# Performance work log

Measured on AMD Instinct MI355X. Metric: run time of the kernel, lower is better.

The kernel has to match this reference:

```python
import jax, jax.numpy as jnp
import numpy as np

N_NODES = 50000
N_EDGES = 800000
IN_FEATS = 32
OUT_FEATS = 32
NUM_HEADS = 4


def setup_inputs() -> dict:
    key = jax.random.key(0)
    ks = jax.random.split(key, 12)
    H, F, IN = NUM_HEADS, OUT_FEATS, IN_FEATS
    h = jax.random.normal(ks[0], (N_NODES, IN), dtype=jnp.float32)
    src = jax.random.randint(ks[1], (N_EDGES,), 0, N_NODES, dtype=jnp.int64)
    dst = jax.random.randint(ks[2], (N_EDGES,), 0, N_NODES, dtype=jnp.int64)
    s = 0.1
    W_gat = jax.random.normal(ks[3], (IN, H * F), dtype=jnp.float32) * s
    attn_l = jax.random.normal(ks[4], (H, F), dtype=jnp.float32) * s
    attn_r = jax.random.normal(ks[5], (H, F), dtype=jnp.float32) * s
    W_ih = jax.random.normal(ks[6], (3 * F, H * F), dtype=jnp.float32) * s
    W_hh = jax.random.normal(ks[7], (3 * F, F), dtype=jnp.float32) * s
    b_ih = jax.random.normal(ks[8], (3 * F,), dtype=jnp.float32) * s
    b_hh = jax.random.normal(ks[9], (3 * F,), dtype=jnp.float32) * s
    return {"h": h, "W_gat": W_gat, "attn_l": attn_l, "attn_r": attn_r,
            "W_ih": W_ih, "W_hh": W_hh, "b_ih": b_ih, "b_hh": b_hh,
            "src": src, "dst": dst}


def reference(h, W_gat, attn_l, attn_r, W_ih, W_hh, b_ih, b_hh, src, dst):
    N = h.shape[0]
    H, F = attn_l.shape
    # --- GATConv ---
    feat = (h @ W_gat).reshape(N, H, F)                      # (N,H,F)
    el = jnp.einsum('nhf,hf->nh', feat, attn_l)              # (N,H)
    er = jnp.einsum('nhf,hf->nh', feat, attn_r)              # (N,H)
    e = jax.nn.leaky_relu(el[src] + er[dst], 0.2)            # (E,H) edge logits
    emax = jax.ops.segment_max(e, dst, num_segments=N)       # per-dst max (stable)
    ee = jnp.exp(e - emax[dst])
    denom = jax.ops.segment_sum(ee, dst, num_segments=N)
    alpha = ee / denom[dst]                                  # segment softmax (E,H)
    msg = feat[src] * alpha[:, :, None]                      # (E,H,F)
    agg = jax.ops.segment_sum(msg, dst, num_segments=N)      # (N,H,F)
    x = agg.reshape(N, H * F)
    # --- GRUCell (torch semantics, gate order r,z,n) ---
    gi = x @ W_ih.T + b_ih                                   # (N,3F)
    gh = h @ W_hh.T + b_hh                                   # (N,3F)
    i_r, i_z, i_n = jnp.split(gi, 3, axis=1)
    h_r, h_z, h_n = jnp.split(gh, 3, axis=1)
    r = jax.nn.sigmoid(i_r + h_r)
    z = jax.nn.sigmoid(i_z + h_z)
    n = jnp.tanh(i_n + r * h_n)
    h_new = (1.0 - z) * n + z * h
    return jax.nn.elu(h_new)
```

## Files before the change

kernel.cpp:

```cpp
#include <hip/hip_runtime.h>
#include <hip/hip_bf16.h>
#include <cmath>

#define N_NODES 50000
#define N_EDGES 800000
#define CAP 64

#define NBINS 196
#define BIN_CAP 8192
#define CUR_PAD 32

#define WCB_ITEMS (144 * 32)
#define WCB_BLOCKS (WCB_ITEMS / 256)
#define WC_ITEMS (192 * 160)
#define WC_BLOCKS (WC_ITEMS / 256)

#define P1_EPT 8
#define P1_EPB (256 * P1_EPT)
#define P1_BLOCKS ((N_EDGES + P1_EPB - 1) / P1_EPB)
#define FEAT_BLOCKS ((N_NODES / 16 + 3) / 4)

typedef __attribute__((ext_vector_type(8))) short bf16x8;
typedef __attribute__((ext_vector_type(4))) float f32x4;

__device__ inline short bfbits(float x) {
    __hip_bfloat16 t = __float2bfloat16(x);
    return *reinterpret_cast<short*>(&t);
}

__device__ inline unsigned char f32_to_fp8(float x) {
    return (unsigned char)(__builtin_amdgcn_cvt_pk_fp8_f32(x, x, 0, false) & 0xff);
}

__global__ __launch_bounds__(256) void k_prep0(
        const float* __restrict__ Wg, const float* __restrict__ al,
        const float* __restrict__ ar, const float* __restrict__ Wih,
        const float* __restrict__ Whh, __hip_bfloat16* __restrict__ Wcomb,
        __hip_bfloat16* __restrict__ Wc, int* __restrict__ bin_cursor) {
    const int t = threadIdx.x;
    if (blockIdx.x < WCB_BLOCKS) {
        const int idx = blockIdx.x * 256 + t;
        const int row = idx >> 5, k = idx & 31;
        float v = 0.f;
        if (row < 128) {
            v = Wg[k * 128 + row];
        } else if (row < 136) {
            const int hd = (row - 128) & 3;
            const float* a = (row < 132) ? (al + hd * 32) : (ar + hd * 32);
            const float* w = Wg + k * 128 + hd * 32;
#pragma unroll
            for (int f = 0; f < 32; ++f) v = fmaf(w[f], a[f], v);
        }
        Wcomb[idx] = __float2bfloat16(v);
        return;
    }
    if (blockIdx.x < WCB_BLOCKS + WC_BLOCKS) {
        const int idx = (blockIdx.x - WCB_BLOCKS) * 256 + t;
        const int r = idx / 160, k = idx - r * 160;
        float v = 0.f;
        if (r < 96) { if (k < 128) v = Wih[r * 128 + k]; }
        else        { if (k >= 128) v = Whh[(r - 96) * 32 + (k - 128)]; }
        Wc[idx] = __float2bfloat16(v);
        return;
    }
    if (t < NBINS) bin_cursor[t * CUR_PAD] = 0;
}

__global__ __launch_bounds__(256) void k_part_feat(
        const float* __restrict__ h, const __hip_bfloat16* __restrict__ Wcomb,
        const int* __restrict__ src, const int* __restrict__ dst,
        int* __restrict__ bin_cursor, unsigned* __restrict__ bin_buf,
        unsigned char* __restrict__ feat, float* __restrict__ el,
        float* __restrict__ er) {
    const int t = threadIdx.x;
    if (blockIdx.x < P1_BLOCKS) {
        __shared__ int bcnt[256], bofs[256], cur[256], gbase[256];
        __shared__ int wt4[4];
        __shared__ unsigned stage[P1_EPB];
        bcnt[t] = 0;
        __syncthreads();
        int bn[P1_EPT];
        unsigned pk[P1_EPT];
        const int ebase = blockIdx.x * P1_EPB + t * P1_EPT;
        if (ebase < N_EDGES) {
            int dd[P1_EPT], ss[P1_EPT];
            *(int4*)(dd)     = *(const int4*)(dst + ebase);
            *(int4*)(dd + 4) = *(const int4*)(dst + ebase + 4);
            *(int4*)(ss)     = *(const int4*)(src + ebase);
            *(int4*)(ss + 4) = *(const int4*)(src + ebase + 4);
#pragma unroll
            for (int q = 0; q < P1_EPT; ++q) {
                bn[q] = dd[q] >> 8;
                pk[q] = (unsigned)ss[q] | ((unsigned)(dd[q] & 255) << 16);
                atomicAdd(&bcnt[bn[q]], 1);
            }
        } else {
#pragma unroll
            for (int q = 0; q < P1_EPT; ++q) bn[q] = -1;
        }
        __syncthreads();
        {
            const int wave = t >> 6, lane = t & 63;
            const int vv = bcnt[t];
            int x = vv;
#pragma unroll
            for (int m = 1; m < 64; m <<= 1) {
                const int y = __shfl_up(x, m, 64);
                if (lane >= m) x += y;
            }
            if (lane == 63) wt4[wave] = x;
            __syncthreads();
            int wb = 0;
#pragma unroll
            for (int i = 0; i < 4; ++i) if (i < wave) wb += wt4[i];
            const int off = wb + x - vv;
            bofs[t] = off;
            cur[t] = off;
            gbase[t] = (vv > 0) ? atomicAdd(&bin_cursor[t * CUR_PAD], vv) : 0;
        }
        __syncthreads();
#pragma unroll
        for (int q = 0; q < P1_EPT; ++q)
            if (bn[q] >= 0) stage[atomicAdd(&cur[bn[q]], 1)] = pk[q];
        __syncthreads();
        if (t < NBINS) {
            const int c = bcnt[t], o = bofs[t], g = gbase[t];
            unsigned* bb = bin_buf + (size_t)t * BIN_CAP;
            for (int j = 0; j < c; ++j) {
                const int gi = g + j;
                if (gi < BIN_CAP) bb[gi] = stage[o + j];
            }
        }
        return;
    }
    __shared__ unsigned char sbuf8[4][16][136];
    const int lane = t & 63, wave = t >> 6;
    const int li = lane & 15, quad = lane >> 4;
    const int mt = (blockIdx.x - P1_BLOCKS) * 4 + wave;
    if (mt >= N_NODES / 16) return;
    const int m_base = mt * 16;
    bf16x8 a;
    {
        const float4* hp = (const float4*)(h + (size_t)(m_base + li) * 32 + quad * 8);
        const float4 f0 = hp[0], f1 = hp[1];
        a[0] = bfbits(f0.x); a[1] = bfbits(f0.y); a[2] = bfbits(f0.z); a[3] = bfbits(f0.w);
        a[4] = bfbits(f1.x); a[5] = bfbits(f1.y); a[6] = bfbits(f1.z); a[7] = bfbits(f1.w);
    }
    f32x4 acc[9];
#pragma unroll
    for (int j = 0; j < 9; ++j) acc[j] = (f32x4){0.f, 0.f, 0.f, 0.f};
#pragma unroll
    for (int j = 0; j < 9; ++j) {
        const bf16x8 b = *(const bf16x8*)(Wcomb + (size_t)(j * 16 + li) * 32 + quad * 8);
        acc[j] = __builtin_amdgcn_mfma_f32_16x16x32_bf16(a, b, acc[j], 0, 0, 0);
    }
#pragma unroll
    for (int j = 0; j < 8; ++j)
#pragma unroll
        for (int i = 0; i < 4; ++i)
            sbuf8[wave][quad * 4 + i][j * 16 + li] = f32_to_fp8(acc[j][i]);
    __builtin_amdgcn_wave_barrier();
#pragma unroll
    for (int rep = 0; rep < 4; ++rep) {
        const int row = rep * 4 + quad;
        const unsigned long long v = *(const unsigned long long*)(&sbuf8[wave][row][li * 8]);
        *(unsigned long long*)(feat + (size_t)(m_base + row) * 128 + li * 8) = v;
    }
    if (li < 8) {
#pragma unroll
        for (int i = 0; i < 4; ++i) {
            const int m = m_base + quad * 4 + i;
            if (li < 4) el[m * 4 + li] = acc[8][i];
            else        er[m * 4 + (li - 4)] = acc[8][i];
        }
    }
}

__global__ __launch_bounds__(256) void k_scat2(
        const int* __restrict__ bin_cursor, const unsigned* __restrict__ bin_buf,
        int* __restrict__ srcs_p, int* __restrict__ counts) {
    __shared__ int lcnt[256];
    const int t = threadIdx.x;
    const int b = blockIdx.x;
    lcnt[t] = 0;
    __syncthreads();
    const int cb = min(bin_cursor[b * CUR_PAD], BIN_CAP);
    const uint4* bb4 = (const uint4*)(bin_buf + (size_t)b * BIN_CAP);
    for (int i = t * 4; i < cb; i += 1024) {
        const uint4 p4 = bb4[i >> 2];
#pragma unroll
        for (int k = 0; k < 4; ++k) {
            if (i + k < cb) {
                const unsigned p = (&p4.x)[k];
                const int dl = p >> 16;
                const int s = p & 0xffff;
                const int pos = atomicAdd(&lcnt[dl], 1);
                if (pos < CAP) srcs_p[(size_t)(b * 256 + dl) * CAP + pos] = s;
            }
        }
    }
    __syncthreads();
    const int node = b * 256 + t;
    if (node < N_NODES) counts[node] = lcnt[t];
}

__global__ __launch_bounds__(256) void k_aggr_gru(
        const int* __restrict__ counts, const int* __restrict__ srcs_p,
        const unsigned char* __restrict__ feat,
        const float* __restrict__ el, const float* __restrict__ er,
        const float* __restrict__ h, const __hip_bfloat16* __restrict__ Wc,
        const float* __restrict__ bih, const float* __restrict__ bhh,
        float* __restrict__ out) {
    __shared__ __hip_bfloat16 xh_tile[16][160];
    __shared__ int   sl_s[4][4][64];
    __shared__ float eel_s[4][256];
    __shared__ float ex[2][3][16][16];
    const int wave = threadIdx.x >> 6;
    const int lane = threadIdx.x & 63;
    float* eel = eel_s[wave];
    const int hs = lane & 3;
    const int eh = lane >> 5;
    const int fl = lane & 31;
    const int hq = fl >> 3;
    const int mbase = blockIdx.x * 16;

    int cnts[4];
#pragma unroll
    for (int u = 0; u < 4; ++u) {
        const int n = mbase + wave * 4 + u;
        cnts[u] = min(counts[n], CAP);
        if (lane < cnts[u]) sl_s[wave][u][lane] = srcs_p[(size_t)n * CAP + lane];
    }
    __builtin_amdgcn_wave_barrier();
    for (int u = 0; u < 4; ++u) {
        const int row = wave * 4 + u;
        const int n = mbase + row;
        const float ern = er[n * 4 + hs];
        const int cnt = cnts[u];
        const int* sl = sl_s[wave][u];
        float a0 = 0.f, a1 = 0.f, a2 = 0.f, a3 = 0.f, psum = 0.f;
#pragma unroll
        for (int p = 0; p < 4; ++p) {
            const int j = p * 64 + lane;
            if (j < cnt * 4) {
                const int s = sl[j >> 2];
                float v = el[s * 4 + hs] + ern;
                v = v > 0.f ? v : 0.2f * v;
                const float e = expf(v);
                eel[j] = e;
                psum += e;
            }
        }
        __builtin_amdgcn_wave_barrier();
        int i = 0;
        for (; i + 8 <= cnt; i += 8) {
            const int s0 = sl[i + eh],     s1 = sl[i + 2 + eh];
            const int s2 = sl[i + 4 + eh], s3 = sl[i + 6 + eh];
            const unsigned u0 = *(const unsigned*)(feat + (size_t)s0 * 128 + fl * 4);
            const unsigned u1 = *(const unsigned*)(feat + (size_t)s1 * 128 + fl * 4);
            const unsigned u2 = *(const unsigned*)(feat + (size_t)s2 * 128 + fl * 4);
            const unsigned u3 = *(const unsigned*)(feat + (size_t)s3 * 128 + fl * 4);
            const float w0 = eel[(i + eh) * 4 + hq];
            const float w1 = eel[(i + 2 + eh) * 4 + hq];
            const float w2 = eel[(i + 4 + eh) * 4 + hq];
            const float w3 = eel[(i + 6 + eh) * 4 + hq];
            a0 = fmaf(w0, __builtin_amdgcn_cvt_f32_fp8(u0, 0), a0);
            a1 = fmaf(w0, __builtin_amdgcn_cvt_f32_fp8(u0, 1), a1);
            a2 = fmaf(w0, __builtin_amdgcn_cvt_f32_fp8(u0, 2), a2);
            a3 = fmaf(w0, __builtin_amdgcn_cvt_f32_fp8(u0, 3), a3);
            a0 = fmaf(w1, __builtin_amdgcn_cvt_f32_fp8(u1, 0), a0);
            a1 = fmaf(w1, __builtin_amdgcn_cvt_f32_fp8(u1, 1), a1);
            a2 = fmaf(w1, __builtin_amdgcn_cvt_f32_fp8(u1, 2), a2);
            a3 = fmaf(w1, __builtin_amdgcn_cvt_f32_fp8(u1, 3), a3);
            a0 = fmaf(w2, __builtin_amdgcn_cvt_f32_fp8(u2, 0), a0);
            a1 = fmaf(w2, __builtin_amdgcn_cvt_f32_fp8(u2, 1), a1);
            a2 = fmaf(w2, __builtin_amdgcn_cvt_f32_fp8(u2, 2), a2);
            a3 = fmaf(w2, __builtin_amdgcn_cvt_f32_fp8(u2, 3), a3);
            a0 = fmaf(w3, __builtin_amdgcn_cvt_f32_fp8(u3, 0), a0);
            a1 = fmaf(w3, __builtin_amdgcn_cvt_f32_fp8(u3, 1), a1);
            a2 = fmaf(w3, __builtin_amdgcn_cvt_f32_fp8(u3, 2), a2);
            a3 = fmaf(w3, __builtin_amdgcn_cvt_f32_fp8(u3, 3), a3);
        }
        for (; i < cnt; i += 2) {
            const int e2 = i + eh;
            if (e2 < cnt) {
                const int s0 = sl[e2];
                const unsigned u0 = *(const unsigned*)(feat + (size_t)s0 * 128 + fl * 4);
                const float w0 = eel[e2 * 4 + hq];
                a0 = fmaf(w0, __builtin_amdgcn_cvt_f32_fp8(u0, 0), a0);
                a1 = fmaf(w0, __builtin_amdgcn_cvt_f32_fp8(u0, 1), a1);
                a2 = fmaf(w0, __builtin_amdgcn_cvt_f32_fp8(u0, 2), a2);
                a3 = fmaf(w0, __builtin_amdgcn_cvt_f32_fp8(u0, 3), a3);
            }
        }
        __builtin_amdgcn_wave_barrier();
        a0 += __shfl_xor(a0, 32, 64);
        a1 += __shfl_xor(a1, 32, 64);
        a2 += __shfl_xor(a2, 32, 64);
        a3 += __shfl_xor(a3, 32, 64);
#pragma unroll
        for (int m = 4; m < 64; m <<= 1) psum += __shfl_xor(psum, m, 64);
        const float dn = __shfl(psum, hq, 64);
        const float inv = (cnt > 0) ? 1.f / dn : 0.f;
        if (lane < 32) {
            __hip_bfloat162 p0, p1;
            p0.x = __float2bfloat16(a0 * inv); p0.y = __float2bfloat16(a1 * inv);
            p1.x = __float2bfloat16(a2 * inv); p1.y = __float2bfloat16(a3 * inv);
            __hip_bfloat162* xp = (__hip_bfloat162*)&xh_tile[row][0];
            xp[lane * 2]     = p0;
            xp[lane * 2 + 1] = p1;
            xh_tile[row][128 + lane] = __float2bfloat16(h[(size_t)n * 32 + lane]);
        }
    }
    __syncthreads();

    const int li = lane & 15, quad = lane >> 4;
    const int cb = wave >> 1;
    const int ghrole = wave & 1;
    bf16x8 a[5];
#pragma unroll
    for (int s = 0; s < 5; ++s)
        a[s] = *(const bf16x8*)((const char*)&xh_tile[0][0] + li * 320 + s * 64 + quad * 16);
    f32x4 acc[3];
#pragma unroll
    for (int g = 0; g < 3; ++g) {
        acc[g] = (f32x4){0.f, 0.f, 0.f, 0.f};
        const int j = g * 2 + cb + ghrole * 6;
        const bf16x8* bp = (const bf16x8*)(Wc + (size_t)(j * 16 + li) * 160 + quad * 8);
        acc[g] = __builtin_amdgcn_mfma_f32_16x16x32_bf16(a[0], bp[0],  acc[g], 0, 0, 0);
        acc[g] = __builtin_amdgcn_mfma_f32_16x16x32_bf16(a[1], bp[4],  acc[g], 0, 0, 0);
        acc[g] = __builtin_amdgcn_mfma_f32_16x16x32_bf16(a[2], bp[8],  acc[g], 0, 0, 0);
        acc[g] = __builtin_amdgcn_mfma_f32_16x16x32_bf16(a[3], bp[12], acc[g], 0, 0, 0);
        acc[g] = __builtin_amdgcn_mfma_f32_16x16x32_bf16(a[4], bp[16], acc[g], 0, 0, 0);
    }
    if (ghrole) {
#pragma unroll
        for (int g = 0; g < 3; ++g)
#pragma unroll
            for (int i = 0; i < 4; ++i)
                ex[cb][g][quad * 4 + i][li] = acc[g][i];
    }
    __syncthreads();
    if (!ghrole) {
        const int c = cb * 16 + li;
        const float bir = bih[c],      bhr = bhh[c];
        const float biz = bih[32 + c], bhz = bhh[32 + c];
        const float bin = bih[64 + c], bhn = bhh[64 + c];
#pragma unroll
        for (int i = 0; i < 4; ++i) {
            const int row = quad * 4 + i;
            const int m = mbase + row;
            const float gr = acc[0][i] + bir + ex[cb][0][row][li] + bhr;
            const float gz = acc[1][i] + biz + ex[cb][1][row][li] + bhz;
            const float r = 1.f / (1.f + expf(-gr));
            const float z = 1.f / (1.f + expf(-gz));
            const float nn = tanhf(acc[2][i] + bin + r * (ex[cb][2][row][li] + bhn));
            const float hv = h[(size_t)m * 32 + c];
            const float hn = (1.f - z) * nn + z * hv;
            out[(size_t)m * 32 + c] = hn > 0.f ? hn : expm1f(hn);
        }
    }
}

extern "C" void kernel_launch(void* const* d_in, const int* in_sizes, int n_in,
                              void* d_out, int out_size, void* d_ws, size_t ws_size,
                              hipStream_t stream) {
    const float* h   = (const float*)d_in[0];
    const float* Wg  = (const float*)d_in[1];
    const float* al  = (const float*)d_in[2];
    const float* ar  = (const float*)d_in[3];
    const float* Wih = (const float*)d_in[4];
    const float* Whh = (const float*)d_in[5];
    const float* bih = (const float*)d_in[6];
    const float* bhh = (const float*)d_in[7];
    const int* src   = (const int*)d_in[8];
    const int* dst   = (const int*)d_in[9];
    float* out = (float*)d_out;

    float* el = (float*)d_ws;
    float* er = el + (size_t)N_NODES * 4;
    unsigned char* feat8 = (unsigned char*)(er + (size_t)N_NODES * 4);
    __hip_bfloat16* Wc    = (__hip_bfloat16*)(feat8 + (size_t)N_NODES * 128);
    __hip_bfloat16* Wcomb = Wc + 192 * 160;
    int* counts  = (int*)(Wcomb + WCB_ITEMS);
    int* srcs_p  = counts + N_NODES;
    int* bin_cursor = srcs_p + (size_t)N_NODES * CAP;
    unsigned* bin_buf = (unsigned*)(bin_cursor + NBINS * CUR_PAD);

    k_prep0<<<WCB_BLOCKS + WC_BLOCKS + 1, 256, 0, stream>>>(
        Wg, al, ar, Wih, Whh, Wcomb, Wc, bin_cursor);
    k_part_feat<<<P1_BLOCKS + FEAT_BLOCKS, 256, 0, stream>>>(
        h, Wcomb, src, dst, bin_cursor, bin_buf, feat8, el, er);
    k_scat2<<<NBINS, 256, 0, stream>>>(bin_cursor, bin_buf, srcs_p, counts);
    k_aggr_gru<<<N_NODES / 16, 256, 0, stream>>>(
        counts, srcs_p, feat8, el, er, h, Wc, bih, bhh, out);
}
```

Measured before the change: 153.1 us.

## Fuse edge softmax weight computation into the gather loop, dropping LDS staging

Instead of a separate pass that computes exp(leaky_relu(el+er)) for each edge and head into shared memory, each lane now computes the weight for its own head inline while gathering features, in chunks of 16 edges with 8 independent loads per lane. The per-wave LDS buffer and the extra wave barrier go away. The denominator now comes from a shuffle reduction over the 8 lanes sharing a head, which counts each weight 8 times and is corrected by the 8/psum scale. In exchange, every lane that shares a head repeats the same exp and el load, and edge counts that are not a multiple of 16 get padded with masked slots.

```diff
diff --git a/kernel.cpp b/kernel.cpp
--- a/kernel.cpp
+++ b/kernel.cpp
@@ -213,12 +213,9 @@
         float* __restrict__ out) {
     __shared__ __hip_bfloat16 xh_tile[16][160];
     __shared__ int   sl_s[4][4][64];
-    __shared__ float eel_s[4][256];
     __shared__ float ex[2][3][16][16];
     const int wave = threadIdx.x >> 6;
     const int lane = threadIdx.x & 63;
-    float* eel = eel_s[wave];
-    const int hs = lane & 3;
     const int eh = lane >> 5;
     const int fl = lane & 31;
     const int hq = fl >> 3;
@@ -235,73 +232,49 @@
     for (int u = 0; u < 4; ++u) {
         const int row = wave * 4 + u;
         const int n = mbase + row;
-        const float ern = er[n * 4 + hs];
         const int cnt = cnts[u];
         const int* sl = sl_s[wave][u];
+        const float ern = er[n * 4 + hq];
         float a0 = 0.f, a1 = 0.f, a2 = 0.f, a3 = 0.f, psum = 0.f;
-#pragma unroll
-        for (int p = 0; p < 4; ++p) {
-            const int j = p * 64 + lane;
-            if (j < cnt * 4) {
-                const int s = sl[j >> 2];
-                float v = el[s * 4 + hs] + ern;
+        for (int i = 0; i < cnt; i += 16) {
+            int  s[8];
+            unsigned uq[8];
+            float w[8];
+#pragma unroll
+            for (int j = 0; j < 8; ++j) {
+                const int e2 = i + 2 * j + eh;
+                s[j] = (e2 < cnt) ? sl[e2] : 0;
+            }
+#pragma unroll
+            for (int j = 0; j < 8; ++j)
+                uq[j] = *(const unsigned*)(feat + (size_t)s[j] * 128 + fl * 4);
+#pragma unroll
+            for (int j = 0; j < 8; ++j)
+                w[j] = el[s[j] * 4 + hq];
+#pragma unroll
+            for (int j = 0; j < 8; ++j) {
+                float v = w[j] + ern;
                 v = v > 0.f ? v : 0.2f * v;
-                const float e = expf(v);
-                eel[j] = e;
-                psum += e;
-            }
-        }
-        __builtin_amdgcn_wave_barrier();
-        int i = 0;
-        for (; i + 8 <= cnt; i += 8) {
-            const int s0 = sl[i + eh],     s1 = sl[i + 2 + eh];
-            const int s2 = sl[i + 4 + eh], s3 = sl[i + 6 + eh];
-            const unsigned u0 = *(const unsigned*)(feat + (size_t)s0 * 128 + fl * 4);
-            const unsigned u1 = *(const unsigned*)(feat + (size_t)s1 * 128 + fl * 4);
-            const unsigned u2 = *(const unsigned*)(feat + (size_t)s2 * 128 + fl * 4);
-            const unsigned u3 = *(const unsigned*)(feat + (size_t)s3 * 128 + fl * 4);
-            const float w0 = eel[(i + eh) * 4 + hq];
-            const float w1 = eel[(i + 2 + eh) * 4 + hq];
-            const float w2 = eel[(i + 4 + eh) * 4 + hq];
-            const float w3 = eel[(i + 6 + eh) * 4 + hq];
-            a0 = fmaf(w0, __builtin_amdgcn_cvt_f32_fp8(u0, 0), a0);
-            a1 = fmaf(w0, __builtin_amdgcn_cvt_f32_fp8(u0, 1), a1);
-            a2 = fmaf(w0, __builtin_amdgcn_cvt_f32_fp8(u0, 2), a2);
-            a3 = fmaf(w0, __builtin_amdgcn_cvt_f32_fp8(u0, 3), a3);
-            a0 = fmaf(w1, __builtin_amdgcn_cvt_f32_fp8(u1, 0), a0);
-            a1 = fmaf(w1, __builtin_amdgcn_cvt_f32_fp8(u1, 1), a1);
-            a2 = fmaf(w1, __builtin_amdgcn_cvt_f32_fp8(u1, 2), a2);
-            a3 = fmaf(w1, __builtin_amdgcn_cvt_f32_fp8(u1, 3), a3);
-            a0 = fmaf(w2, __builtin_amdgcn_cvt_f32_fp8(u2, 0), a0);
-            a1 = fmaf(w2, __builtin_amdgcn_cvt_f32_fp8(u2, 1), a1);
-            a2 = fmaf(w2, __builtin_amdgcn_cvt_f32_fp8(u2, 2), a2);
-            a3 = fmaf(w2, __builtin_amdgcn_cvt_f32_fp8(u2, 3), a3);
-            a0 = fmaf(w3, __builtin_amdgcn_cvt_f32_fp8(u3, 0), a0);
-            a1 = fmaf(w3, __builtin_amdgcn_cvt_f32_fp8(u3, 1), a1);
-            a2 = fmaf(w3, __builtin_amdgcn_cvt_f32_fp8(u3, 2), a2);
-            a3 = fmaf(w3, __builtin_amdgcn_cvt_f32_fp8(u3, 3), a3);
-        }
-        for (; i < cnt; i += 2) {
-            const int e2 = i + eh;
-            if (e2 < cnt) {
-                const int s0 = sl[e2];
-                const unsigned u0 = *(const unsigned*)(feat + (size_t)s0 * 128 + fl * 4);
-                const float w0 = eel[e2 * 4 + hq];
-                a0 = fmaf(w0, __builtin_amdgcn_cvt_f32_fp8(u0, 0), a0);
-                a1 = fmaf(w0, __builtin_amdgcn_cvt_f32_fp8(u0, 1), a1);
-                a2 = fmaf(w0, __builtin_amdgcn_cvt_f32_fp8(u0, 2), a2);
-                a3 = fmaf(w0, __builtin_amdgcn_cvt_f32_fp8(u0, 3), a3);
-            }
-        }
-        __builtin_amdgcn_wave_barrier();
+                w[j] = (i + 2 * j + eh < cnt) ? __expf(v) : 0.f;
+                psum += w[j];
+            }
+#pragma unroll
+            for (int j = 0; j < 8; ++j) {
+                a0 = fmaf(w[j], __builtin_amdgcn_cvt_f32_fp8(uq[j], 0), a0);
+                a1 = fmaf(w[j], __builtin_amdgcn_cvt_f32_fp8(uq[j], 1), a1);
+                a2 = fmaf(w[j], __builtin_amdgcn_cvt_f32_fp8(uq[j], 2), a2);
+                a3 = fmaf(w[j], __builtin_amdgcn_cvt_f32_fp8(uq[j], 3), a3);
+            }
+        }
         a0 += __shfl_xor(a0, 32, 64);
         a1 += __shfl_xor(a1, 32, 64);
         a2 += __shfl_xor(a2, 32, 64);
         a3 += __shfl_xor(a3, 32, 64);
-#pragma unroll
-        for (int m = 4; m < 64; m <<= 1) psum += __shfl_xor(psum, m, 64);
-        const float dn = __shfl(psum, hq, 64);
-        const float inv = (cnt > 0) ? 1.f / dn : 0.f;
+        psum += __shfl_xor(psum, 1, 64);
+        psum += __shfl_xor(psum, 2, 64);
+        psum += __shfl_xor(psum, 4, 64);
+        psum += __shfl_xor(psum, 32, 64);
+        const float inv = (cnt > 0) ? 8.f / psum : 0.f;
         if (lane < 32) {
             __hip_bfloat162 p0, p1;
             p0.x = __float2bfloat16(a0 * inv); p0.y = __float2bfloat16(a1 * inv);
```

New measurement: 151.5 us. About the same (-1.1%).
